# Optimization experiments

Measured on AMD Instinct MI355X. Metric: run time of the kernel, lower is better.

Reference implementation:

```python
import jax, jax.numpy as jnp
import numpy as np

K = 3
STRIDE = 1
PAD = 1


def _unfold(x, k, stride, pad):
    # x: (B, C, H, W) -> (B, C*k*k, L) matching torch.nn.functional.unfold
    # ordering: channel slowest, then kh, then kw.
    B, C, H, W = x.shape
    Hout = (H + 2 * pad - k) // stride + 1
    Wout = (W + 2 * pad - k) // stride + 1
    xp = jnp.pad(x, ((0, 0), (0, 0), (pad, pad), (pad, pad)))
    patches = []  # fixed k*k loop (9 iters), not a data-dim loop
    for i in range(k):
        for j in range(k):
            patches.append(xp[:, :, i:i + stride * Hout:stride, j:j + stride * Wout:stride])
    # (B, C, k*k, Hout, Wout) -> (B, C*k*k, L)
    p = jnp.stack(patches, axis=2)
    return p.reshape(B, C * k * k, Hout * Wout), Hout, Wout


def setup_inputs() -> dict:
    key = jax.random.key(0)
    k1, k2 = jax.random.split(key)
    x = jax.random.normal(k1, (4, 32, 56, 56), dtype=jnp.float32)
    weights = jax.random.normal(k2, (64, 32, 3, 3), dtype=jnp.float32)
    return {"x": x, "weights": weights}


def reference(x, weights):
    B = x.shape[0]
    O = weights.shape[0]
    mu_w = jnp.mean(jnp.abs(weights))
    x_unf, Hout, Wout = _unfold(x, K, STRIDE, PAD)      # (B, Ckk, L)
    w_unf = weights.reshape(O, -1)                        # (O, Ckk)
    # min-plus 'convolution': broadcast min then reduce over patch dim
    min_val = jnp.minimum(x_unf[:, None, :, :], w_unf[None, :, :, None])  # (B, O, Ckk, L)
    z = mu_w * jnp.sum(min_val, axis=2)                   # (B, O, L)
    return z.reshape(B, O, Hout, Wout)
```

## Files before the change

### kernel.cpp

```cpp
#include <hip/hip_runtime.h>

#define CIN  32
#define OCH  64
#define HH   56
#define WW   56
#define BB   4
#define OT   4
#define IMG  (HH * WW)
#define NW   18432
#define PH   58
#define PW   58
#define PIMG (PH * PW)
#define NXPK (BB * (CIN/2) * PIMG)
#define XPKBLKS (NXPK / 256)
#define NWPK (OCH * (CIN/2) * 9)
#define WPKBLKS (NWPK / 256)
#define WOFFu 64
#define XOFFu (WOFFu + NWPK)

typedef _Float16 h2 __attribute__((ext_vector_type(2)));

__global__ __launch_bounds__(256) void prep(const float* __restrict__ x,
                                            const float* __restrict__ w,
                                            float* __restrict__ ws) {
    unsigned* wsu = reinterpret_cast<unsigned*>(ws);
    if (blockIdx.x < XPKBLKS) {
        int idx = blockIdx.x * 256 + threadIdx.x;
        int bc  = idx / PIMG;
        int r   = idx - bc * PIMG;
        int ph  = r / PW;
        int pw  = r - ph * PW;
        int hh  = ph - 1, wc = pw - 1;
        float v0 = 0.f, v1 = 0.f;
        if ((unsigned)hh < (unsigned)HH && (unsigned)wc < (unsigned)WW) {
            int base = ((bc >> 4) * CIN + (bc & 15) * 2) * IMG + hh * WW + wc;
            v0 = x[base];
            v1 = x[base + IMG];
        }
        h2 p; p.x = (_Float16)v0; p.y = (_Float16)v1;
        wsu[XOFFu + idx] = __builtin_bit_cast(unsigned, p);
        return;
    }
    if (blockIdx.x < XPKBLKS + WPKBLKS) {
        int idx = (blockIdx.x - XPKBLKS) * 256 + threadIdx.x;
        int t    = idx % 9;
        int rest = idx / 9;
        int cp   = rest & 15;
        int oo   = rest >> 4;
        int base = oo * (CIN * 9) + cp * 18 + t;
        h2 p; p.x = (_Float16)w[base]; p.y = (_Float16)w[base + 9];
        wsu[WOFFu + idx] = __builtin_bit_cast(unsigned, p);
        return;
    }
    float s = 0.f;
    const float4* w4 = reinterpret_cast<const float4*>(w);
    #pragma unroll
    for (int k = 0; k < 18; ++k) {
        float4 v = w4[k * 256 + threadIdx.x];
        s += fabsf(v.x) + fabsf(v.y) + fabsf(v.z) + fabsf(v.w);
    }
    #pragma unroll
    for (int off = 32; off; off >>= 1) s += __shfl_down(s, off);
    __shared__ float sm[4];
    if ((threadIdx.x & 63) == 0) sm[threadIdx.x >> 6] = s;
    __syncthreads();
    if (threadIdx.x == 0)
        ws[0] = (sm[0] + sm[1] + sm[2] + sm[3]) * (1.0f / (float)NW);
}

__global__ __launch_bounds__(128) void minconv_kernel(const float* __restrict__ ws,
                                                      const float* __restrict__ wts,
                                                      float* __restrict__ out) {
    const unsigned* wsu = reinterpret_cast<const unsigned*>(ws);
    const int lane = threadIdx.x & 63;
    const int wv   = threadIdx.x >> 6;
    const int wvs  = __builtin_amdgcn_readfirstlane(wv);
    const int hw = blockIdx.x * 64 + lane;
    const int o0 = blockIdx.y * OT;
    const int b  = blockIdx.z;
    const int h  = hw / WW;
    const int w  = hw - h * WW;

    const float mu = ws[0];

    const int cp0 = wvs * 8;
    const unsigned* xq = wsu + XOFFu + (size_t)(b * 16 + cp0) * PIMG + h * PW + w;
    const unsigned* wq = wsu + WOFFu;

    h2 ones; ones.x = (_Float16)1.f; ones.y = (_Float16)1.f;
    float acc0 = 0.f, acc1 = 0.f, acc2 = 0.f, acc3 = 0.f;

    #pragma unroll
    for (int cp = 0; cp < 8; ++cp) {
        h2 xv[9];
        #pragma unroll
        for (int kh = 0; kh < 3; ++kh)
            #pragma unroll
            for (int kw = 0; kw < 3; ++kw)
                xv[kh * 3 + kw] = __builtin_bit_cast(h2, xq[cp * PIMG + kh * PW + kw]);
        #pragma unroll
        for (int oo = 0; oo < OT; ++oo) {
            const int wbase = ((o0 + oo) * 16 + (cp0 + cp)) * 9;
            float a = 0.f;
            #pragma unroll
            for (int t = 0; t < 9; ++t) {
                h2 wp = __builtin_bit_cast(h2, wq[wbase + t]);
                h2 m  = __builtin_elementwise_min(xv[t], wp);
                a = __builtin_amdgcn_fdot2(m, ones, a, false);
            }
            switch (oo) {
                case 0: acc0 += a; break;
                case 1: acc1 += a; break;
                case 2: acc2 += a; break;
                case 3: acc3 += a; break;
            }
        }
    }

    __shared__ float red[2][2][64];
    if (wv == 0) {
        red[0][0][lane] = acc2;
        red[0][1][lane] = acc3;
    } else {
        red[1][0][lane] = acc0;
        red[1][1][lane] = acc1;
    }
    __syncthreads();

    float* ob = out + ((size_t)b * OCH + o0) * IMG + hw;
    if (wv == 0) {
        ob[0]       = mu * (acc0 + red[1][0][lane]);
        ob[IMG]     = mu * (acc1 + red[1][1][lane]);
    } else {
        ob[2 * IMG] = mu * (acc2 + red[0][0][lane]);
        ob[3 * IMG] = mu * (acc3 + red[0][1][lane]);
    }
}

extern "C" void kernel_launch(void* const* d_in, const int* in_sizes, int n_in,
                              void* d_out, int out_size, void* d_ws, size_t ws_size,
                              hipStream_t stream) {
    const float* x   = (const float*)d_in[0];
    const float* w   = (const float*)d_in[1];
    float*       out = (float*)d_out;
    float*       ws  = (float*)d_ws;

    prep<<<XPKBLKS + WPKBLKS + 1, 256, 0, stream>>>(x, w, ws);
    dim3 grid(IMG / 64, OCH / OT, BB);
    minconv_kernel<<<grid, 128, 0, stream>>>(ws, w, out);
}
```

Before: 73.29 us.

## Stage per-tile weights in LDS, split channels across four waves

The packed weights are reordered so each output tile's 576 words are contiguous and interleaved by output channel. Each block copies its tile's weights into shared memory and reads them as uint4 vectors covering four output channels. The block grows to 256 threads, with each wave taking 4 channel pairs, and the partial sums are combined through a 4-way shared-memory reduction. An inline-asm v_pk_min_f16 replaces the builtin min. This aims to cut scalar/global weight loads and raise per-block parallelism, at the cost of an extra barrier and a larger reduction.

After: 67.79 us. 1.08x faster.

```diff
diff --git a/kernel.cpp b/kernel.cpp
--- a/kernel.cpp
+++ b/kernel.cpp
@@ -19,6 +19,13 @@
 #define XOFFu (WOFFu + NWPK)
 
 typedef _Float16 h2 __attribute__((ext_vector_type(2)));
+
+static __device__ __forceinline__ h2 pkmin_vv(h2 xv, unsigned wu) {
+    unsigned xu = __builtin_bit_cast(unsigned, xv);
+    unsigned ru;
+    asm("v_pk_min_f16 %0, %1, %2" : "=v"(ru) : "v"(xu), "v"(wu));
+    return __builtin_bit_cast(h2, ru);
+}
 
 __global__ __launch_bounds__(256) void prep(const float* __restrict__ x,
                                             const float* __restrict__ w,
@@ -43,12 +50,18 @@
     }
     if (blockIdx.x < XPKBLKS + WPKBLKS) {
         int idx = (blockIdx.x - XPKBLKS) * 256 + threadIdx.x;
-        int t    = idx % 9;
-        int rest = idx / 9;
-        int cp   = rest & 15;
-        int oo   = rest >> 4;
-        int base = oo * (CIN * 9) + cp * 18 + t;
-        h2 p; p.x = (_Float16)w[base]; p.y = (_Float16)w[base + 9];
+        int otile = idx / 576;
+        int r     = idx - otile * 576;
+        int wv4   = r / 144;
+        int r2    = r - wv4 * 144;
+        int cl    = r2 / 36;
+        int r3    = r2 - cl * 36;
+        int t     = r3 >> 2;
+        int oo    = r3 & 3;
+        int o     = otile * OT + oo;
+        int cp    = wv4 * 4 + cl;
+        int src   = o * (CIN * 9) + cp * 18 + t;
+        h2 p; p.x = (_Float16)w[src]; p.y = (_Float16)w[src + 9];
         wsu[WOFFu + idx] = __builtin_bit_cast(unsigned, p);
         return;
     }
@@ -68,12 +81,13 @@
         ws[0] = (sm[0] + sm[1] + sm[2] + sm[3]) * (1.0f / (float)NW);
 }
 
-__global__ __launch_bounds__(128) void minconv_kernel(const float* __restrict__ ws,
+__global__ __launch_bounds__(256) void minconv_kernel(const float* __restrict__ ws,
                                                       const float* __restrict__ wts,
                                                       float* __restrict__ out) {
     const unsigned* wsu = reinterpret_cast<const unsigned*>(ws);
-    const int lane = threadIdx.x & 63;
-    const int wv   = threadIdx.x >> 6;
+    const int tid  = threadIdx.x;
+    const int lane = tid & 63;
+    const int wv   = tid >> 6;
     const int wvs  = __builtin_amdgcn_readfirstlane(wv);
     const int hw = blockIdx.x * 64 + lane;
     const int o0 = blockIdx.y * OT;
@@ -83,58 +97,57 @@
 
     const float mu = ws[0];
 
-    const int cp0 = wvs * 8;
+    __shared__ __align__(16) unsigned wlds[576];
+    __shared__ float red[4][4][64];
+
+    {
+        const unsigned* wt = wsu + WOFFu + blockIdx.y * 576;
+        *reinterpret_cast<uint2*>(&wlds[tid * 2]) =
+            *reinterpret_cast<const uint2*>(&wt[tid * 2]);
+        if (tid < 64) wlds[512 + tid] = wt[512 + tid];
+    }
+
+    const int cp0 = wvs * 4;
     const unsigned* xq = wsu + XOFFu + (size_t)(b * 16 + cp0) * PIMG + h * PW + w;
-    const unsigned* wq = wsu + WOFFu;
+
+    __syncthreads();
 
     h2 ones; ones.x = (_Float16)1.f; ones.y = (_Float16)1.f;
-    float acc0 = 0.f, acc1 = 0.f, acc2 = 0.f, acc3 = 0.f;
+    float a0 = 0.f, a1 = 0.f, a2 = 0.f, a3 = 0.f;
+    const unsigned* wl = wlds + wv * 144;
 
     #pragma unroll
-    for (int cp = 0; cp < 8; ++cp) {
+    for (int cl = 0; cl < 4; ++cl) {
         h2 xv[9];
         #pragma unroll
         for (int kh = 0; kh < 3; ++kh)
             #pragma unroll
             for (int kw = 0; kw < 3; ++kw)
-                xv[kh * 3 + kw] = __builtin_bit_cast(h2, xq[cp * PIMG + kh * PW + kw]);
+                xv[kh * 3 + kw] =
+                    __builtin_bit_cast(h2, xq[cl * PIMG + kh * PW + kw]);
         #pragma unroll
-        for (int oo = 0; oo < OT; ++oo) {
-            const int wbase = ((o0 + oo) * 16 + (cp0 + cp)) * 9;
-            float a = 0.f;
-            #pragma unroll
-            for (int t = 0; t < 9; ++t) {
-                h2 wp = __builtin_bit_cast(h2, wq[wbase + t]);
-                h2 m  = __builtin_elementwise_min(xv[t], wp);
-                a = __builtin_amdgcn_fdot2(m, ones, a, false);
-            }
-            switch (oo) {
-                case 0: acc0 += a; break;
-                case 1: acc1 += a; break;
-                case 2: acc2 += a; break;
-                case 3: acc3 += a; break;
-            }
+        for (int t = 0; t < 9; ++t) {
+            uint4 q = *reinterpret_cast<const uint4*>(&wl[cl * 36 + t * 4]);
+            h2 m0 = pkmin_vv(xv[t], q.x);
+            a0 = __builtin_amdgcn_fdot2(m0, ones, a0, false);
+            h2 m1 = pkmin_vv(xv[t], q.y);
+            a1 = __builtin_amdgcn_fdot2(m1, ones, a1, false);
+            h2 m2 = pkmin_vv(xv[t], q.z);
+            a2 = __builtin_amdgcn_fdot2(m2, ones, a2, false);
+            h2 m3 = pkmin_vv(xv[t], q.w);
+            a3 = __builtin_amdgcn_fdot2(m3, ones, a3, false);
         }
     }
 
-    __shared__ float red[2][2][64];
-    if (wv == 0) {
-        red[0][0][lane] = acc2;
-        red[0][1][lane] = acc3;
-    } else {
-        red[1][0][lane] = acc0;
-        red[1][1][lane] = acc1;
-    }
+    red[wv][0][lane] = a0;
+    red[wv][1][lane] = a1;
+    red[wv][2][lane] = a2;
+    red[wv][3][lane] = a3;
     __syncthreads();
 
-    float* ob = out + ((size_t)b * OCH + o0) * IMG + hw;
-    if (wv == 0) {
-        ob[0]       = mu * (acc0 + red[1][0][lane]);
-        ob[IMG]     = mu * (acc1 + red[1][1][lane]);
-    } else {
-        ob[2 * IMG] = mu * (acc2 + red[0][0][lane]);
-        ob[3 * IMG] = mu * (acc3 + red[0][1][lane]);
-    }
+    float s = red[0][wv][lane] + red[1][wv][lane]
+            + red[2][wv][lane] + red[3][wv][lane];
+    out[((size_t)b * OCH + o0 + wv) * IMG + hw] = mu * s;
 }
 
 extern "C" void kernel_launch(void* const* d_in, const int* in_sizes, int n_in,
@@ -147,5 +160,5 @@
 
     prep<<<XPKBLKS + WPKBLKS + 1, 256, 0, stream>>>(x, w, ws);
     dim3 grid(IMG / 64, OCH / OT, BB);
-    minconv_kernel<<<grid, 128, 0, stream>>>(ws, w, out);
+    minconv_kernel<<<grid, 256, 0, stream>>>(ws, w, out);
 }
```
